# Performance work log

Hardware: AMD Instinct MI355X
Metric: run time of the kernel (lower is better)

Reference implementation:

```python
import jax, jax.numpy as jnp
from jax import lax
import numpy as np

N, C, H, W = 16, 128, 128, 128
CH = C // 4  # adapter contraction channels


def setup_inputs() -> dict:
    key = jax.random.key(0)
    ks = jax.random.split(key, 12)
    x = jax.random.normal(ks[0], (N, C, H, W), jnp.float32)
    # intensity in {1,2,3} as the torch module expects (intensity[i]-1 indexes adapters)
    intensity = jax.random.randint(ks[1], (N,), 1, 4)
    conv1_w = jax.random.normal(ks[2], (C, C, 3, 3), jnp.float32) * 0.02
    conv1_b = jnp.zeros((C,), jnp.float32)
    prelu1 = jnp.float32(0.25)  # nn.PReLU default single shared slope
    conv2_w = jax.random.normal(ks[3], (C, C, 3, 3), jnp.float32) * 0.02
    conv2_b = jnp.zeros((C,), jnp.float32)
    # 3 adapter experts, stacked on leading axis
    aW1 = jax.random.normal(ks[4], (3, CH, C), jnp.float32) * 0.05
    ab1 = jnp.zeros((3, CH), jnp.float32)
    aW2 = jax.random.normal(ks[5], (3, C, CH), jnp.float32) * 0.05
    ab2 = jnp.zeros((3, C), jnp.float32)
    prelu2 = jnp.float32(0.25)
    return dict(x=x, intensity=intensity, conv1_w=conv1_w, conv1_b=conv1_b,
                prelu1=prelu1, conv2_w=conv2_w, conv2_b=conv2_b,
                aW1=aW1, ab1=ab1, aW2=aW2, ab2=ab2, prelu2=prelu2)


def prelu(x, a):
    return jnp.where(x >= 0, x, a * x)


def conv3x3(x, w, b):
    y = lax.conv_general_dilated(x, w, window_strides=(1, 1),
                                 padding=((1, 1), (1, 1)),
                                 dimension_numbers=('NCHW', 'OIHW', 'NCHW'))
    return y + b[None, :, None, None]


def reference(x, intensity, conv1_w, conv1_b, prelu1, conv2_w, conv2_b,
              aW1, ab1, aW2, ab2, prelu2):
    h = prelu(conv3x3(x, conv1_w, conv1_b), prelu1)      # conv1 + PReLU
    h = conv3x3(h, conv2_w, conv2_b)                     # conv2, no activation
    x1 = jnp.mean(h, axis=(2, 3))                        # AdaptiveAvgPool2d(1)+Flatten -> [N,C]
    idx = intensity - 1                                  # expert id per sample
    W1, b1 = aW1[idx], ab1[idx]                          # gather per-sample expert weights
    W2, b2 = aW2[idx], ab2[idx]
    a = jax.nn.relu(jnp.einsum('nc,nhc->nh', x1, W1) + b1)
    g = jnp.einsum('nh,nch->nc', a, W2) + b2             # [N,C]
    out = h * jax.nn.sigmoid(g)[:, :, None, None] + x    # gated residual
    return prelu(out, prelu2)
```

## Files before the change

kernel.cpp:

```cpp
#include <hip/hip_runtime.h>
#include <hip/hip_bf16.h>
#include <math.h>

#define NN   16
#define C_   128
#define HH   128
#define WW   128
#define CHID 32
#define NTILES 64

#define BCHUNK 33792

typedef short bf16x8 __attribute__((ext_vector_type(8)));
typedef float f32x4  __attribute__((ext_vector_type(4)));

__device__ inline void glds16(const void* g, void* l) {
    __builtin_amdgcn_global_load_lds(
        (const __attribute__((address_space(1))) unsigned int*)g,
        (__attribute__((address_space(3))) unsigned int*)l, 16, 0, 0);
}

__device__ inline unsigned short f2bf(float f) {
    __hip_bfloat16 h = __float2bfloat16(f);
    return *reinterpret_cast<unsigned short*>(&h);
}

__global__ __launch_bounds__(64) void pack_w_k(
    const float* __restrict__ w1, const float* __restrict__ w2,
    unsigned short* __restrict__ wl)
{
    const int b = blockIdx.x;
    const int conv = b / 288, rem = b % 288;
    const int kk = rem / 32, ck = (rem % 32) / 8, cot = rem % 8;
    const int l = threadIdx.x;
    const int co  = cot * 16 + (l & 15);
    const int ci0 = ck * 32 + (l >> 4) * 8;
    const float* W = conv ? w2 : w1;
    union { unsigned short u[8]; uint4 v; } pk;
#pragma unroll
    for (int j = 0; j < 8; ++j)
        pk.u[j] = f2bf(W[(size_t)(co * C_ + ci0 + j) * 9 + kk]);
    unsigned short* dst = wl + (size_t)conv * 147456 +
        ((((size_t)kk * 4 + ck) * 8 + cot) * 64 + l) * 8;
    *reinterpret_cast<uint4*>(dst) = pk.v;
}

__global__ __launch_bounds__(256) void to_cnhwc_k(
    const float* __restrict__ x, unsigned short* __restrict__ xb)
{
    __shared__ unsigned short s_t[128][136];
    const int y = blockIdx.x, n = blockIdx.y, t = threadIdx.x;

#pragma unroll
    for (int p = 0; p < 16; ++p) {
        int fi = p * 256 + t;
        int ci = fi >> 5, x0 = (fi & 31) * 4;
        float4 v = *reinterpret_cast<const float4*>(
            x + (((size_t)(n * C_ + ci) * HH) + y) * WW + x0);
        const int slot = ((ci >> 3) ^ ((x0 >> 2) & 7)) * 8 + (ci & 7);
        s_t[x0 + 0][slot] = f2bf(v.x);
        s_t[x0 + 1][slot] = f2bf(v.y);
        s_t[x0 + 2][slot] = f2bf(v.z);
        s_t[x0 + 3][slot] = f2bf(v.w);
    }
    __syncthreads();
    unsigned short* dstbase = xb + ((size_t)(n * HH + y)) * 16384;
#pragma unroll
    for (int p = 0; p < 8; ++p) {
        int o = p * 256 + t;
        int sl = o >> 8, u = o & 255;
        int xc = u >> 1, q = u & 1;
        int oct = sl * 2 + q;
        uint4 v = *reinterpret_cast<const uint4*>(
            &s_t[xc][(oct ^ ((xc >> 2) & 7)) * 8]);
        *reinterpret_cast<uint4*>(dstbase + (size_t)sl * 2048 + xc * 16 + q * 8) = v;
    }
}

template<int MODE>
__global__ __launch_bounds__(512) void conv_mfma_k(
    const unsigned short* __restrict__ inb,
    const unsigned short* __restrict__ wl,
    const float* __restrict__ bias,
    const float* __restrict__ prelu_a,
    unsigned short* __restrict__ outb,
    float* __restrict__ outf,
    float* __restrict__ partial)
{
    __shared__ char  smem[2 * BCHUNK];
    __shared__ float s_part[8][64];

    const int tid = threadIdx.x;
    const int l = tid & 63, w = tid >> 6;
    const int wco = w >> 2, wy = (w >> 1) & 1, wxh = w & 1;
    const int lg = l >> 4, l15 = l & 15;
    const int yp = blockIdx.x, n = blockIdx.z;
    const int y0 = yp * 2;
    const int rot = (yp + n) & 3;

    const f32x4 fz = {0.f, 0.f, 0.f, 0.f};
    f32x4 acc[4][4];
#pragma unroll
    for (int m = 0; m < 4; ++m)
#pragma unroll
        for (int nf = 0; nf < 4; ++nf) acc[m][nf] = fz;

    const bf16x8* wv = reinterpret_cast<const bf16x8*>(wl);
    const uint4 z4 = {0u, 0u, 0u, 0u};

    auto stage = [&](int ck, char* sb) {
        const int r = w >> 1, xh = w & 1;
        const int ygl = y0 - 1 + r;
        if (ygl < 0 || ygl >= HH) {
            int t2 = xh * 64 + l;
            for (int i = t2; i < 528; i += 128)
                *reinterpret_cast<uint4*>(sb + r * 8448 + i * 16) = z4;
        } else {
            if (xh == 0 && l < 8) {
                int col = (l < 4) ? 0 : 129, q = l & 3;
                *reinterpret_cast<uint4*>(sb + r * 8448 + col * 64 + q * 16) = z4;
            }
            const size_t rowbase = ((size_t)(n * HH + ygl)) * 32768;
#pragma unroll
            for (int i = 0; i < 4; ++i) {
                const int p  = xh * 64 + i * 16 + (l >> 2);
                const int sd = (l & 3) ^ (((1 + p) >> 1) & 3);
                const char* g = (const char*)inb + rowbase +
                    (size_t)(2 * ck + (sd >> 1)) * 4096 + p * 32 + (sd & 1) * 16;
                glds16(g, sb + r * 8448 + (1 + xh * 64 + i * 16) * 64);
            }
        }
    };

    stage(rot, smem);
    __syncthreads();

    for (int c8 = 0; c8 < 4; ++c8) {
        const int ck = (c8 + rot) & 3;
        char* buf = smem + (c8 & 1) * BCHUNK;
        if (c8 < 3) stage((c8 + 1 + rot) & 3, smem + ((c8 + 1) & 1) * BCHUNK);

        auto loadA = [&](int kk, bf16x8* a) {
#pragma unroll
            for (int m = 0; m < 4; ++m)
                a[m] = wv[(((size_t)kk * 4 + ck) * 8 + wco * 4 + m) * 64 + l];
        };
        auto rdB = [&](int kk, bf16x8* b) {
            const int ky = kk / 3, kx = kk % 3;
            const int rrow = wy + ky;
#pragma unroll
            for (int nf = 0; nf < 4; ++nf) {
                int xi = wxh * 64 + nf * 16 + l15 + kx;
                int slot = lg ^ ((xi >> 1) & 3);
                b[nf] = *reinterpret_cast<const bf16x8*>(
                    buf + rrow * 8448 + xi * 64 + slot * 16);
            }
        };

        bf16x8 ap[3][4], bp[2][4];
        loadA(0, ap[0]);
        loadA(1, ap[1]);
        rdB(0, bp[0]);
#pragma unroll
        for (int kk = 0; kk < 9; ++kk) {
            if (kk < 7) loadA(kk + 2, ap[(kk + 2) % 3]);
            if (kk < 8) rdB(kk + 1, bp[(kk + 1) & 1]);
            bf16x8* ac = ap[kk % 3];
            bf16x8* bc = bp[kk & 1];
#pragma unroll
            for (int nf = 0; nf < 4; ++nf)
#pragma unroll
                for (int m = 0; m < 4; ++m)
                    acc[m][nf] = __builtin_amdgcn_mfma_f32_16x16x32_bf16(
                        ac[m], bc[nf], acc[m][nf], 0, 0, 0);
        }
        __syncthreads();
    }

    const int ybase = y0 + wy;
    if (MODE == 0 || MODE == 1) {
        const float a1 = (MODE == 0) ? *prelu_a : 0.f;
        float ps[4][4];
        if (MODE == 1) {
#pragma unroll
            for (int m = 0; m < 4; ++m)
#pragma unroll
                for (int jj = 0; jj < 4; ++jj) ps[m][jj] = 0.f;
        }
        unsigned short (*s_rp)[136] = reinterpret_cast<unsigned short (*)[136]>(smem);
        for (int r = 0; r < 2; ++r) {
            if (wy == r) {
#pragma unroll
                for (int m = 0; m < 4; ++m) {
                    const int co0 = wco * 64 + m * 16 + lg * 4;
#pragma unroll
                    for (int nf = 0; nf < 4; ++nf) {
                        const int xc = wxh * 64 + nf * 16 + l15;
                        union { unsigned short u[4]; uint2 v; } pk;
#pragma unroll
                        for (int jj = 0; jj < 4; ++jj) {
                            float f = acc[m][nf][jj] + bias[co0 + jj];
                            if (MODE == 0) f = (f >= 0.f) ? f : a1 * f;
                            else           ps[m][jj] += f;
                            pk.u[jj] = f2bf(f);
                        }
                        *reinterpret_cast<uint2*>(&s_rp[xc][co0]) = pk.v;
                    }
                }
            }
            __syncthreads();
            const int y = y0 + r;
#pragma unroll
            for (int p = 0; p < 4; ++p) {
                int u = p * 512 + tid;
                int xc = u >> 4, k = u & 15;
                uint4 v = *reinterpret_cast<const uint4*>(&s_rp[xc][k * 8]);
                *reinterpret_cast<uint4*>(outb +
                    (((size_t)(n * HH + y)) * 8 + (k >> 1)) * 2048 +
                    xc * 16 + (k & 1) * 8) = v;
            }
            __syncthreads();
        }
        if (MODE == 1) {
#pragma unroll
            for (int m = 0; m < 4; ++m)
#pragma unroll
                for (int jj = 0; jj < 4; ++jj) {
                    float s = ps[m][jj];
                    s += __shfl_xor(s, 1); s += __shfl_xor(s, 2);
                    s += __shfl_xor(s, 4); s += __shfl_xor(s, 8);
                    ps[m][jj] = s;
                }
            if (l15 == 0) {
#pragma unroll
                for (int m = 0; m < 4; ++m)
#pragma unroll
                    for (int jj = 0; jj < 4; ++jj)
                        s_part[w][m * 16 + lg * 4 + jj] = ps[m][jj];
            }
            __syncthreads();
            if (tid < C_) {
                const int half = tid >> 6;
                float s = 0.f;
#pragma unroll
                for (int w2 = 0; w2 < 4; ++w2) s += s_part[half * 4 + w2][tid & 63];
                partial[((size_t)(n * C_ + tid)) * NTILES + yp] = s;
            }
        }
    } else {
        float ps[4][4];
#pragma unroll
        for (int m = 0; m < 4; ++m)
#pragma unroll
            for (int jj = 0; jj < 4; ++jj) ps[m][jj] = 0.f;
#pragma unroll
        for (int m = 0; m < 4; ++m) {
            const int co0 = wco * 64 + m * 16 + lg * 4;
#pragma unroll
            for (int nf = 0; nf < 4; ++nf) {
                const int xc = wxh * 64 + nf * 16 + l15;
#pragma unroll
                for (int jj = 0; jj < 4; ++jj) {
                    float f = acc[m][nf][jj] + bias[co0 + jj];
                    outf[(((size_t)(n * C_ + co0 + jj)) * HH + ybase) * WW + xc] = f;
                    ps[m][jj] += f;
                }
            }
        }
#pragma unroll
        for (int m = 0; m < 4; ++m)
#pragma unroll
            for (int jj = 0; jj < 4; ++jj) {
                float s = ps[m][jj];
                s += __shfl_xor(s, 1); s += __shfl_xor(s, 2);
                s += __shfl_xor(s, 4); s += __shfl_xor(s, 8);
                ps[m][jj] = s;
            }
        if (l15 == 0) {
#pragma unroll
            for (int m = 0; m < 4; ++m)
#pragma unroll
                for (int jj = 0; jj < 4; ++jj)
                    s_part[w][m * 16 + lg * 4 + jj] = ps[m][jj];
        }
        __syncthreads();
        if (tid < C_) {
            const int half = tid >> 6;
            float s = 0.f;
#pragma unroll
            for (int w2 = 0; w2 < 4; ++w2) s += s_part[half * 4 + w2][tid & 63];
            partial[((size_t)(n * C_ + tid)) * NTILES + yp] = s;
        }
    }
}

__global__ __launch_bounds__(C_) void adapter_k(
    const float* __restrict__ partial, const int* __restrict__ intensity,
    const float* __restrict__ aW1, const float* __restrict__ ab1,
    const float* __restrict__ aW2, const float* __restrict__ ab2,
    float* __restrict__ sig)
{
    __shared__ float sx[C_];
    __shared__ float sa[CHID];
    const int n = blockIdx.x, c = threadIdx.x;

    float s = 0.f;
    for (int t = 0; t < NTILES; ++t)
        s += partial[(size_t)(n * C_ + c) * NTILES + t];
    sx[c] = s * (1.f / (float)(HH * WW));
    __syncthreads();

    const int idx = intensity[n] - 1;
    if (c < CHID) {
        float a = ab1[idx * CHID + c];
        const float* wrow = aW1 + (size_t)(idx * CHID + c) * C_;
        for (int k = 0; k < C_; ++k) a = fmaf(wrow[k], sx[k], a);
        sa[c] = fmaxf(a, 0.f);
    }
    __syncthreads();

    float g = ab2[idx * C_ + c];
    const float* w2row = aW2 + (size_t)(idx * C_ + c) * CHID;
#pragma unroll
    for (int k = 0; k < CHID; ++k) g = fmaf(w2row[k], sa[k], g);
    sig[n * C_ + c] = 1.f / (1.f + expf(-g));
}

__global__ __launch_bounds__(256) void epilogue_bf16_k(
    const unsigned short* __restrict__ h2b, const float* __restrict__ x,
    const float* __restrict__ sig, const float* __restrict__ prelu_a,
    float* __restrict__ out)
{
    __shared__ unsigned short s_h[128][136];
    const int y = blockIdx.x, n = blockIdx.y, t = threadIdx.x;
    const float a = *prelu_a;
    const unsigned short* slab = h2b + ((size_t)(n * HH + y)) * 16384;

#pragma unroll
    for (int p = 0; p < 8; ++p) {
        int o = p * 256 + t;
        int sl = o >> 8, u = o & 255;
        int xc = u >> 1, q = u & 1;
        int oct = sl * 2 + q;
        uint4 v = *reinterpret_cast<const uint4*>(
            slab + (size_t)sl * 2048 + xc * 16 + q * 8);
        *reinterpret_cast<uint4*>(&s_h[xc][(oct ^ ((xc >> 2) & 7)) * 8]) = v;
    }
    __syncthreads();

#pragma unroll
    for (int p = 0; p < 16; ++p) {
        int fi = p * 256 + t;
        int ci = fi >> 5, x0 = (fi & 31) * 4;
        const float sg = sig[n * C_ + ci];
        float4 x4 = *reinterpret_cast<const float4*>(
            x + (((size_t)(n * C_ + ci)) * HH + y) * WW + x0);
        float4 v;
        float hv[4];
#pragma unroll
        for (int j = 0; j < 4; ++j) {
            int xr = x0 + j;
            unsigned short hu = s_h[xr][((ci >> 3) ^ ((xr >> 2) & 7)) * 8 + (ci & 7)];
            unsigned int bits = ((unsigned int)hu) << 16;
            hv[j] = *reinterpret_cast<float*>(&bits);
        }
        v.x = hv[0] * sg + x4.x;  v.x = (v.x >= 0.f) ? v.x : a * v.x;
        v.y = hv[1] * sg + x4.y;  v.y = (v.y >= 0.f) ? v.y : a * v.y;
        v.z = hv[2] * sg + x4.z;  v.z = (v.z >= 0.f) ? v.z : a * v.z;
        v.w = hv[3] * sg + x4.w;  v.w = (v.w >= 0.f) ? v.w : a * v.w;
        *reinterpret_cast<float4*>(
            out + (((size_t)(n * C_ + ci)) * HH + y) * WW + x0) = v;
    }
}

__global__ __launch_bounds__(256) void epilogue_k(
    const float* __restrict__ x, const float* __restrict__ sig,
    const float* __restrict__ prelu_a, float* __restrict__ out, int total4)
{
    const float a = *prelu_a;
    const int stride = gridDim.x * blockDim.x;
    for (int i = blockIdx.x * blockDim.x + threadIdx.x; i < total4; i += stride) {
        const int nc = (i * 4) >> 14;
        const float s = sig[nc];
        float4 h4 = ((const float4*)out)[i];
        float4 x4 = ((const float4*)x)[i];
        float4 v;
        v.x = h4.x * s + x4.x;  v.x = (v.x >= 0.f) ? v.x : a * v.x;
        v.y = h4.y * s + x4.y;  v.y = (v.y >= 0.f) ? v.y : a * v.y;
        v.z = h4.z * s + x4.z;  v.z = (v.z >= 0.f) ? v.z : a * v.z;
        v.w = h4.w * s + x4.w;  v.w = (v.w >= 0.f) ? v.w : a * v.w;
        ((float4*)out)[i] = v;
    }
}

extern "C" void kernel_launch(void* const* d_in, const int* in_sizes, int n_in,
                              void* d_out, int out_size, void* d_ws, size_t ws_size,
                              hipStream_t stream)
{
    const float* x         = (const float*)d_in[0];
    const int*   intensity = (const int*)  d_in[1];
    const float* w1        = (const float*)d_in[2];
    const float* b1        = (const float*)d_in[3];
    const float* p1        = (const float*)d_in[4];
    const float* w2        = (const float*)d_in[5];
    const float* b2        = (const float*)d_in[6];
    const float* aW1       = (const float*)d_in[7];
    const float* ab1       = (const float*)d_in[8];
    const float* aW2       = (const float*)d_in[9];
    const float* ab2       = (const float*)d_in[10];
    const float* p2        = (const float*)d_in[11];
    float* out = (float*)d_out;

    const size_t SLAB = (size_t)33554432 * 2;
    const size_t WLB  = (size_t)294912 * 2;
    const size_t NEED = 2 * SLAB + WLB + (size_t)(NN * C_ * NTILES + NN * C_ + 64) * 4;
    const bool big = ws_size >= NEED;

    unsigned short* h1b = (unsigned short*)d_ws;
    unsigned short* xb;
    unsigned short* h2b = nullptr;
    unsigned short* wl;
    if (big) {
        xb  = (unsigned short*)((char*)d_ws + SLAB);
        h2b = xb;
        wl  = (unsigned short*)((char*)d_ws + 2 * SLAB);
    } else {
        xb  = (unsigned short*)d_out;
        wl  = (unsigned short*)((char*)d_ws + SLAB);
    }
    float* partial = (float*)((char*)wl + WLB);
    float* sig     = partial + (size_t)NN * C_ * NTILES;

    pack_w_k<<<dim3(576), dim3(64), 0, stream>>>(w1, w2, wl);
    to_cnhwc_k<<<dim3(HH, NN), dim3(256), 0, stream>>>(x, xb);

    conv_mfma_k<0><<<dim3(NTILES, 1, NN), dim3(512), 0, stream>>>(
        xb, wl, b1, p1, h1b, nullptr, nullptr);

    if (big) {
        conv_mfma_k<1><<<dim3(NTILES, 1, NN), dim3(512), 0, stream>>>(
            h1b, wl + (size_t)147456, b2, nullptr, h2b, nullptr, partial);
        adapter_k<<<dim3(NN), dim3(C_), 0, stream>>>(
            partial, intensity, aW1, ab1, aW2, ab2, sig);
        epilogue_bf16_k<<<dim3(HH, NN), dim3(256), 0, stream>>>(
            h2b, x, sig, p2, out);
    } else {
        conv_mfma_k<2><<<dim3(NTILES, 1, NN), dim3(512), 0, stream>>>(
            h1b, wl + (size_t)147456, b2, nullptr, nullptr, out, partial);
        adapter_k<<<dim3(NN), dim3(C_), 0, stream>>>(
            partial, intensity, aW1, ab1, aW2, ab2, sig);
        const int total4 = NN * C_ * HH * WW / 4;
        epilogue_k<<<dim3(2048), dim3(256), 0, stream>>>(x, sig, p2, out, total4);
    }
}
```

Before: 272.1 us.

## Restructure conv MFMA main loop with explicit barriers, waitcnt and priority scheduling

Rewrites the implicit-GEMM conv inner loop so each of the nine taps is a barrier-delimited phase. Waves sync together, use manual s_waitcnt (vmcnt(8) to let the next chunk's global->LDS loads stay in flight), and raise priority with s_setprio around the MFMA cluster. Weight prefetch drops from two taps ahead to one, and the B fragments are now read per tap instead of double-buffered. The aim is lockstep MFMA/memory interleaving across waves, at the cost of many extra barriers per chunk and reliance on the hand-tuned vmcnt count being correct.

Result: slower. 287.6 us (+5.7%).

```diff
diff --git a/kernel.cpp b/kernel.cpp
--- a/kernel.cpp
+++ b/kernel.cpp
@@ -132,22 +132,33 @@
         }
     };
 
+    auto loadA = [&](int kk, int ck, bf16x8* a) {
+#pragma unroll
+        for (int m = 0; m < 4; ++m)
+            a[m] = wv[(((size_t)kk * 4 + ck) * 8 + wco * 4 + m) * 64 + l];
+    };
+
     stage(rot, smem);
-    __syncthreads();
+
+    bf16x8 ap[2][4];
 
     for (int c8 = 0; c8 < 4; ++c8) {
         const int ck = (c8 + rot) & 3;
-        char* buf = smem + (c8 & 1) * BCHUNK;
-        if (c8 < 3) stage((c8 + 1 + rot) & 3, smem + ((c8 + 1) & 1) * BCHUNK);
-
-        auto loadA = [&](int kk, bf16x8* a) {
-#pragma unroll
-            for (int m = 0; m < 4; ++m)
-                a[m] = wv[(((size_t)kk * 4 + ck) * 8 + wco * 4 + m) * 64 + l];
-        };
-        auto rdB = [&](int kk, bf16x8* b) {
+        char* buf  = smem + (c8 & 1) * BCHUNK;
+        char* nbuf = smem + ((c8 + 1) & 1) * BCHUNK;
+
+        if (c8 == 0) asm volatile("s_waitcnt vmcnt(0) lgkmcnt(0)" ::: "memory");
+        else         asm volatile("s_waitcnt vmcnt(8) lgkmcnt(0)" ::: "memory");
+        __builtin_amdgcn_sched_barrier(0);
+        __builtin_amdgcn_s_barrier();
+
+        loadA(0, ck, ap[0]);
+
+#pragma unroll
+        for (int kk = 0; kk < 9; ++kk) {
             const int ky = kk / 3, kx = kk % 3;
             const int rrow = wy + ky;
+            bf16x8 b[4];
 #pragma unroll
             for (int nf = 0; nf < 4; ++nf) {
                 int xi = wxh * 64 + nf * 16 + l15 + kx;
@@ -155,27 +166,27 @@
                 b[nf] = *reinterpret_cast<const bf16x8*>(
                     buf + rrow * 8448 + xi * 64 + slot * 16);
             }
-        };
-
-        bf16x8 ap[3][4], bp[2][4];
-        loadA(0, ap[0]);
-        loadA(1, ap[1]);
-        rdB(0, bp[0]);
-#pragma unroll
-        for (int kk = 0; kk < 9; ++kk) {
-            if (kk < 7) loadA(kk + 2, ap[(kk + 2) % 3]);
-            if (kk < 8) rdB(kk + 1, bp[(kk + 1) & 1]);
-            bf16x8* ac = ap[kk % 3];
-            bf16x8* bc = bp[kk & 1];
+            if (kk < 8) loadA(kk + 1, ck, ap[(kk + 1) & 1]);
+            if (kk == 0 && c8 < 3) stage((c8 + 1 + rot) & 3, nbuf);
+
+            __builtin_amdgcn_sched_barrier(0);
+            __builtin_amdgcn_s_barrier();
+            asm volatile("s_waitcnt lgkmcnt(0)" ::: "memory");
+            __builtin_amdgcn_sched_barrier(0);
+            __builtin_amdgcn_s_setprio(1);
+            bf16x8* ac = ap[kk & 1];
 #pragma unroll
             for (int nf = 0; nf < 4; ++nf)
 #pragma unroll
                 for (int m = 0; m < 4; ++m)
                     acc[m][nf] = __builtin_amdgcn_mfma_f32_16x16x32_bf16(
-                        ac[m], bc[nf], acc[m][nf], 0, 0, 0);
-        }
-        __syncthreads();
-    }
+                        ac[m], b[nf], acc[m][nf], 0, 0, 0);
+            __builtin_amdgcn_s_setprio(0);
+            __builtin_amdgcn_sched_barrier(0);
+            __builtin_amdgcn_s_barrier();
+        }
+    }
+    __syncthreads();
 
     const int ybase = y0 + wy;
     if (MODE == 0 || MODE == 1) {
```
